# Performance work log

Measured on AMD Instinct MI355X. Metric: run time of the kernel, lower is better.

The kernel has to match this reference:

```python
import jax, jax.numpy as jnp
import numpy as np

B, T, D, N = 8, 2048, 1024, 256


def setup_inputs() -> dict:
    key = jax.random.key(0)
    ks = jax.random.split(key, 6)
    sD = 1.0 / np.sqrt(D)
    sN = 1.0 / np.sqrt(N)
    return {
        "x": jax.random.normal(ks[0], (B, T, D), dtype=jnp.float32),
        "Wa": jax.random.normal(ks[1], (D, N), dtype=jnp.float32) * sD,
        "ba": jnp.zeros((N,), jnp.float32),
        "Wb": jax.random.normal(ks[2], (D, N), dtype=jnp.float32) * sD,
        "bb": jnp.zeros((N,), jnp.float32),
        "Wc": jax.random.normal(ks[3], (D, N), dtype=jnp.float32) * sD,
        "bc": jnp.zeros((N,), jnp.float32),
        "Wd": jax.random.normal(ks[4], (D, D), dtype=jnp.float32) * sD,
        "bd": jnp.zeros((D,), jnp.float32),
        "Wy": jax.random.normal(ks[5], (N, D), dtype=jnp.float32) * sN,
        "by": jnp.zeros((D,), jnp.float32),
    }


def reference(x, Wa, ba, Wb, bb, Wc, bc, Wd, bd, Wy, by):
    # Precompute all input-dependent gates/projections in batched GEMMs.
    a = jax.nn.sigmoid(jnp.einsum("btd,dn->btn", x, Wa) + ba)  # (B,T,N)
    b = jnp.einsum("btd,dn->btn", x, Wb) + bb                   # (B,T,N)
    c = jnp.tanh(jnp.einsum("btd,dn->btn", x, Wc) + bc)          # (B,T,N)
    d = jnp.einsum("btd,de->bte", x, Wd) + bd                    # (B,T,D)

    # Sequential linear-gated recurrence: s_t = a_t*s_{t-1} + (1-a_t)*b_t
    def step(s, abc):
        at, bt, ct = abc
        s = at * s + (1.0 - at) * bt
        return s, ct * s

    aT = jnp.swapaxes(a, 0, 1)  # (T,B,N)
    bT = jnp.swapaxes(b, 0, 1)
    cT = jnp.swapaxes(c, 0, 1)
    s0 = jnp.zeros((x.shape[0], Wa.shape[1]), x.dtype)
    _, csT = jax.lax.scan(step, s0, (aT, bT, cT))  # (T,B,N)
    cs = jnp.swapaxes(csT, 0, 1)                    # (B,T,N)

    # Output projection applied once over the full sequence.
    y = jnp.einsum("btn,nd->btd", cs, Wy) + by + d  # (B,T,D)
    return y
```

## Files before the change

kernel.cpp:

```cpp
#include <hip/hip_runtime.h>
#include <hip/hip_bf16.h>

typedef unsigned short u16;
typedef __attribute__((ext_vector_type(8))) short bf16x8;
typedef __attribute__((ext_vector_type(4))) float f32x4;

#define AS1 __attribute__((address_space(1)))
#define AS3 __attribute__((address_space(3)))

#define Bx 8
#define Tt 2048
#define Dd 1024
#define Nn 256
#define Mm (Bx*Tt)
#define CHAINS (Bx*Nn)
#define NCH 32
#define TC 64
#define NCOMB 1792

#define WS_NEED 105644032u

#define CVT_BLOCKS (Mm*Dd/4/256)
#define PACK_BLOCKS (32*32*5)

__device__ __forceinline__ u16 f2bf(float f) {
  union { float f; unsigned u; } v; v.f = f;
  unsigned u = v.u;
  u += 0x7fffu + ((u >> 16) & 1u);
  return (u16)(u >> 16);
}

__device__ __forceinline__ float bf2f(u16 h) {
  union { unsigned u; float f; } v; v.u = ((unsigned)h) << 16;
  return v.f;
}

__device__ __forceinline__ void gload_lds16(const void* g, void* l) {
  __builtin_amdgcn_global_load_lds((AS1 void*)(g), (AS3 void*)(l), 16, 0, 0);
}

__global__ void prep_kernel(const float* __restrict__ x, u16* __restrict__ xb,
                            const float* __restrict__ Wa, const float* __restrict__ Wb,
                            const float* __restrict__ Wc, const float* __restrict__ Wd,
                            const float* __restrict__ Wy,
                            u16* __restrict__ Wcomb, u16* __restrict__ Wyt) {
  const int bid = blockIdx.x;
  if (bid < CVT_BLOCKS) {
    int i = bid * blockDim.x + threadIdx.x;
    float4 v = ((const float4*)x)[i];
    unsigned lo = (unsigned)f2bf(v.x) | ((unsigned)f2bf(v.y) << 16);
    unsigned hi = (unsigned)f2bf(v.z) | ((unsigned)f2bf(v.w) << 16);
    ((uint2*)xb)[i] = make_uint2(lo, hi);
    return;
  }
  __shared__ float tile[32][33];
  const int pid = bid - CVT_BLOCKS;
  const int z = pid >> 10;
  const int rem = pid & 1023;
  const int bx = rem & 31, by = rem >> 5;
  const float* src; u16* dst; int R, C, dld;
  if (z < 3)       { src = (z==0?Wa:(z==1?Wb:Wc)); dst = Wcomb + (size_t)z*256*1024; R=1024; C=256;  dld=1024; }
  else if (z == 3) { src = Wd; dst = Wcomb + (size_t)768*1024; R=1024; C=1024; dld=1024; }
  else             { src = Wy; dst = Wyt; R=256;  C=1024; dld=256;  }
  int c0 = bx * 32, r0 = by * 32;
  if (c0 >= C || r0 >= R) return;
  int tx = threadIdx.x & 31, ty = threadIdx.x >> 5;
  #pragma unroll
  for (int i = 0; i < 32; i += 8)
    tile[ty + i][tx] = src[(size_t)(r0 + ty + i)*C + (c0 + tx)];
  __syncthreads();
  #pragma unroll
  for (int i = 0; i < 32; i += 8) {
    int c = c0 + ty + i, r = r0 + tx;
    dst[(size_t)c*dld + r] = f2bf(tile[tx][ty + i]);
  }
}

template<int EPI>
__global__ __launch_bounds__(512, 4) void gemm_bt_kernel(
    const u16* __restrict__ A, const u16* __restrict__ Bt, int K, int gx,
    u16* __restrict__ outA, float* __restrict__ outO, u16* __restrict__ dtmp,
    const float* __restrict__ b0, const float* __restrict__ b1,
    const float* __restrict__ b2, const float* __restrict__ b3) {
  __shared__ u16 ldsA[256*64];
  __shared__ u16 ldsB[128*64];
  const int tid = threadIdx.x;
  const int lane = tid & 63, wid = tid >> 6;
  const int wm = wid >> 1, wn = wid & 1;

  const int h = blockIdx.x;
  const int id = (h & 7) * (gridDim.x >> 3) + (h >> 3);
  const int mt = id / gx, nt = id % gx;
  const int m0 = mt * 256, n0 = nt * 128;

  f32x4 acc[4][4] = {};

  const int rl  = tid >> 3;
  const int ssl = (tid & 7) ^ (rl & 7);

  auto stage = [&](int k0) {
    #pragma unroll
    for (int u = 0; u < 4; ++u)
      gload_lds16(A + (size_t)(m0 + u*64 + rl)*K + k0 + ssl*8,
                  ldsA + u*4096 + tid*8);
    #pragma unroll
    for (int u = 0; u < 2; ++u)
      gload_lds16(Bt + (size_t)(n0 + u*64 + rl)*K + k0 + ssl*8,
                  ldsB + u*4096 + tid*8);
  };

  const int lr = lane & 15, kq = lane >> 4, sw = lane & 7;
  const int arow = wm*64 + lr;
  const int brow = wn*64 + lr;

  for (int k0 = 0; k0 < K; k0 += 64) {
    stage(k0);
    __syncthreads();
    #pragma unroll
    for (int kk = 0; kk < 2; ++kk) {
      const int q = ((kk*4 + kq) ^ sw) * 8;
      bf16x8 af[4], bfr[4];
      #pragma unroll
      for (int mi = 0; mi < 4; ++mi)
        af[mi]  = *(const bf16x8*)&ldsA[(arow + mi*16)*64 + q];
      #pragma unroll
      for (int ni = 0; ni < 4; ++ni)
        bfr[ni] = *(const bf16x8*)&ldsB[(brow + ni*16)*64 + q];
      __builtin_amdgcn_s_setprio(1);
      #pragma unroll
      for (int mi = 0; mi < 4; ++mi)
        #pragma unroll
        for (int ni = 0; ni < 4; ++ni)
          acc[mi][ni] = __builtin_amdgcn_mfma_f32_16x16x32_bf16(af[mi], bfr[ni], acc[mi][ni], 0, 0, 0);
      __builtin_amdgcn_s_setprio(0);
    }
    __syncthreads();
  }

  const int crow = m0 + wm*64 + (lane >> 4)*4;
  const int ccol = wn*64 + (lane & 15);
  #pragma unroll
  for (int mi = 0; mi < 4; ++mi) {
    #pragma unroll
    for (int ni = 0; ni < 4; ++ni) {
      int coln = n0 + ccol + ni*16;
      #pragma unroll
      for (int r = 0; r < 4; ++r) {
        int row = crow + mi*16 + r;
        float v = acc[mi][ni][r];
        if (EPI == 0) {
          if (coln < 768) {
            int seg = coln >> 8, cn = coln & 255;
            if (seg == 0)      v = 1.f / (1.f + __expf(-(v + b0[cn])));
            else if (seg == 1) v = v + b1[cn];
            else               v = tanhf(v + b2[cn]);
            outA[(size_t)row*768 + coln] = f2bf(v);
          } else {
            int col = coln - 768;
            if (dtmp) dtmp[(size_t)row*1024 + col] = f2bf(v + b3[col]);
            else      outO[(size_t)row*1024 + col] = v + b3[col];
          }
        } else {
          const size_t o = (size_t)row*1024 + coln;
          if (dtmp) outO[o] = v + b0[coln] + bf2f(dtmp[o]);
          else      outO[o] = outO[o] + v + b0[coln];
        }
      }
    }
  }
}

__global__ void scanA_kernel(const u16* __restrict__ abc,
                             float* __restrict__ Asum, float* __restrict__ Usum) {
  int idx = blockIdx.x * blockDim.x + threadIdx.x;
  int chain = idx & (CHAINS - 1);
  int ch = idx >> 11;
  int bb = chain >> 8, n = chain & 255;
  const u16* base = abc + (size_t)(bb*Tt + ch*TC) * 768;
  float A = 1.f, U = 0.f;
  for (int t = 0; t < TC; ++t) {
    float a = bf2f(base[(size_t)t*768 + n]);
    float b = bf2f(base[(size_t)t*768 + 256 + n]);
    U = a*U + (1.f - a)*b;
    A *= a;
  }
  Asum[idx] = A; Usum[idx] = U;
}

__global__ void scanB_kernel(const float* __restrict__ Asum, const float* __restrict__ Usum,
                             float* __restrict__ Spre) {
  int chain = blockIdx.x * blockDim.x + threadIdx.x;
  float s = 0.f;
  for (int ch = 0; ch < NCH; ++ch) {
    int i = (ch << 11) + chain;
    Spre[i] = s;
    s = Asum[i]*s + Usum[i];
  }
}

__global__ void scanC_kernel(const u16* __restrict__ abc, const float* __restrict__ Spre,
                             u16* __restrict__ cs) {
  int idx = blockIdx.x * blockDim.x + threadIdx.x;
  int chain = idx & (CHAINS - 1);
  int ch = idx >> 11;
  int bb = chain >> 8, n = chain & 255;
  const u16* base = abc + (size_t)(bb*Tt + ch*TC) * 768;
  u16* csb = cs + (size_t)(bb*Tt + ch*TC) * 256 + n;
  float s = Spre[idx];
  for (int t = 0; t < TC; ++t) {
    float a = bf2f(base[(size_t)t*768 + n]);
    float b = bf2f(base[(size_t)t*768 + 256 + n]);
    float c = bf2f(base[(size_t)t*768 + 512 + n]);
    s = a*s + (1.f - a)*b;
    csb[(size_t)t*256] = f2bf(c*s);
  }
}

extern "C" void kernel_launch(void* const* d_in, const int* in_sizes, int n_in,
                              void* d_out, int out_size, void* d_ws, size_t ws_size,
                              hipStream_t stream) {
  const float* x  = (const float*)d_in[0];
  const float* Wa = (const float*)d_in[1];
  const float* ba = (const float*)d_in[2];
  const float* Wb = (const float*)d_in[3];
  const float* bb = (const float*)d_in[4];
  const float* Wc = (const float*)d_in[5];
  const float* bc = (const float*)d_in[6];
  const float* Wd = (const float*)d_in[7];
  const float* bd = (const float*)d_in[8];
  const float* Wy = (const float*)d_in[9];
  const float* by = (const float*)d_in[10];
  float* out = (float*)d_out;
  char* ws = (char*)d_ws;

  u16*  xb    = (u16*) (ws + 0);
  u16*  Wcomb = (u16*) (ws + 33554432);
  u16*  Wyt   = (u16*) (ws + 37224448);
  u16*  abcb  = (u16*) (ws + 37748736);
  u16*  cs    = (u16*) (ws + 62914560);
  float* Asum = (float*)(ws + 71303168);
  float* Usum = (float*)(ws + 71565312);
  float* Spre = (float*)(ws + 71827456);
  u16*  dtmp  = (ws_size >= WS_NEED) ? (u16*)(ws + 72089600) : nullptr;

  prep_kernel<<<CVT_BLOCKS + PACK_BLOCKS, 256, 0, stream>>>(
      x, xb, Wa, Wb, Wc, Wd, Wy, Wcomb, Wyt);
  gemm_bt_kernel<0><<<896, 512, 0, stream>>>(
      xb, Wcomb, Dd, NCOMB/128, abcb, out, dtmp, ba, bb, bc, bd);
  scanA_kernel<<<CHAINS*NCH/256, 256, 0, stream>>>(abcb, Asum, Usum);
  scanB_kernel<<<CHAINS/256, 256, 0, stream>>>(Asum, Usum, Spre);
  scanC_kernel<<<CHAINS*NCH/256, 256, 0, stream>>>(abcb, Spre, cs);
  gemm_bt_kernel<2><<<512, 512, 0, stream>>>(
      cs, Wyt, Nn, Dd/128, nullptr, out, dtmp, by, nullptr, nullptr, nullptr);
}
```

Before: 154.5 us.

## Double-buffer GEMM LDS tiles with 128x128 blocks and prefetch overlap

Block tiles in the bf16 GEMM shrink from 256x128 with 512 threads to 128x128 with 256 threads. LDS is double-buffered so the next K-slice is fetched by global_load_lds while MFMAs run on the current slice, and each iteration ends with explicit vmcnt waits and barriers. The goal is to hide global-load latency and cut the two syncthreads per K step. The cost is more blocks, which means more redundant B-tile traffic and a different occupancy mix.

```diff
diff --git a/kernel.cpp b/kernel.cpp
--- a/kernel.cpp
+++ b/kernel.cpp
@@ -22,6 +22,10 @@
 
 #define CVT_BLOCKS (Mm*Dd/4/256)
 #define PACK_BLOCKS (32*32*5)
+
+#define VMCNT0 asm volatile("s_waitcnt vmcnt(0)" ::: "memory")
+#define BARR   __builtin_amdgcn_s_barrier()
+#define SCHEDB __builtin_amdgcn_sched_barrier(0)
 
 __device__ __forceinline__ u16 f2bf(float f) {
   union { float f; unsigned u; } v; v.f = f;
@@ -77,55 +81,65 @@
 }
 
 template<int EPI>
-__global__ __launch_bounds__(512, 4) void gemm_bt_kernel(
+__global__ __launch_bounds__(256, 4) void gemm_bt_kernel(
     const u16* __restrict__ A, const u16* __restrict__ Bt, int K, int gx,
     u16* __restrict__ outA, float* __restrict__ outO, u16* __restrict__ dtmp,
     const float* __restrict__ b0, const float* __restrict__ b1,
     const float* __restrict__ b2, const float* __restrict__ b3) {
-  __shared__ u16 ldsA[256*64];
-  __shared__ u16 ldsB[128*64];
+  __shared__ u16 ldsA[2*128*64];
+  __shared__ u16 ldsB[2*128*64];
   const int tid = threadIdx.x;
   const int lane = tid & 63, wid = tid >> 6;
-  const int wm = wid >> 1, wn = wid & 1;
+  const int wr = wid >> 1, wc = wid & 1;
 
   const int h = blockIdx.x;
   const int id = (h & 7) * (gridDim.x >> 3) + (h >> 3);
   const int mt = id / gx, nt = id % gx;
-  const int m0 = mt * 256, n0 = nt * 128;
+  const int m0 = mt * 128, n0 = nt * 128;
+  const int NT = K >> 6;
 
   f32x4 acc[4][4] = {};
 
-  const int rl  = tid >> 3;
-  const int ssl = (tid & 7) ^ (rl & 7);
-
-  auto stage = [&](int k0) {
+  const int srow = lane >> 3;
+  const int sq   = (lane & 7) ^ srow;
+
+  auto stage = [&](int b, int t) {
+    const int k0 = t << 6;
     #pragma unroll
-    for (int u = 0; u < 4; ++u)
-      gload_lds16(A + (size_t)(m0 + u*64 + rl)*K + k0 + ssl*8,
-                  ldsA + u*4096 + tid*8);
-    #pragma unroll
-    for (int u = 0; u < 2; ++u)
-      gload_lds16(Bt + (size_t)(n0 + u*64 + rl)*K + k0 + ssl*8,
-                  ldsB + u*4096 + tid*8);
+    for (int i = 0; i < 4; ++i) {
+      int g = wid*4 + i;
+      int r = g*8 + srow;
+      gload_lds16(A + (size_t)(m0 + r)*K + k0 + sq*8, (char*)ldsA + b*16384 + g*1024);
+      gload_lds16(Bt + (size_t)(n0 + r)*K + k0 + sq*8, (char*)ldsB + b*16384 + g*1024);
+    }
   };
 
-  const int lr = lane & 15, kq = lane >> 4, sw = lane & 7;
-  const int arow = wm*64 + lr;
-  const int brow = wn*64 + lr;
-
-  for (int k0 = 0; k0 < K; k0 += 64) {
-    stage(k0);
-    __syncthreads();
+  const int kq  = lane >> 4;
+  const int swz = lane & 7;
+  const int arow = wr*64 + (lane & 15);
+  const int brow = wc*64 + (lane & 15);
+
+  stage(0, 0);
+  VMCNT0;
+  BARR; SCHEDB;
+
+  for (int t = 0; t < NT; ++t) {
+    const int cur = t & 1;
+    const int cb  = cur * 8192;
+
+    if (t + 1 < NT) stage(cur ^ 1, t + 1);
+    SCHEDB;
+
     #pragma unroll
     for (int kk = 0; kk < 2; ++kk) {
-      const int q = ((kk*4 + kq) ^ sw) * 8;
+      const int q = ((kk*4 + kq) ^ swz) * 8;
       bf16x8 af[4], bfr[4];
       #pragma unroll
       for (int mi = 0; mi < 4; ++mi)
-        af[mi]  = *(const bf16x8*)&ldsA[(arow + mi*16)*64 + q];
+        af[mi]  = *(const bf16x8*)&ldsA[cb + (arow + mi*16)*64 + q];
       #pragma unroll
       for (int ni = 0; ni < 4; ++ni)
-        bfr[ni] = *(const bf16x8*)&ldsB[(brow + ni*16)*64 + q];
+        bfr[ni] = *(const bf16x8*)&ldsB[cb + (brow + ni*16)*64 + q];
       __builtin_amdgcn_s_setprio(1);
       #pragma unroll
       for (int mi = 0; mi < 4; ++mi)
@@ -134,11 +148,13 @@
           acc[mi][ni] = __builtin_amdgcn_mfma_f32_16x16x32_bf16(af[mi], bfr[ni], acc[mi][ni], 0, 0, 0);
       __builtin_amdgcn_s_setprio(0);
     }
-    __syncthreads();
-  }
-
-  const int crow = m0 + wm*64 + (lane >> 4)*4;
-  const int ccol = wn*64 + (lane & 15);
+
+    VMCNT0;
+    BARR; SCHEDB;
+  }
+
+  const int crow = m0 + wr*64 + (lane >> 4)*4;
+  const int ccol = wc*64 + (lane & 15);
   #pragma unroll
   for (int mi = 0; mi < 4; ++mi) {
     #pragma unroll
@@ -245,11 +261,11 @@
 
   prep_kernel<<<CVT_BLOCKS + PACK_BLOCKS, 256, 0, stream>>>(
       x, xb, Wa, Wb, Wc, Wd, Wy, Wcomb, Wyt);
-  gemm_bt_kernel<0><<<896, 512, 0, stream>>>(
+  gemm_bt_kernel<0><<<1792, 256, 0, stream>>>(
       xb, Wcomb, Dd, NCOMB/128, abcb, out, dtmp, ba, bb, bc, bd);
   scanA_kernel<<<CHAINS*NCH/256, 256, 0, stream>>>(abcb, Asum, Usum);
   scanB_kernel<<<CHAINS/256, 256, 0, stream>>>(Asum, Usum, Spre);
   scanC_kernel<<<CHAINS*NCH/256, 256, 0, stream>>>(abcb, Spre, cs);
-  gemm_bt_kernel<2><<<512, 512, 0, stream>>>(
+  gemm_bt_kernel<2><<<1024, 256, 0, stream>>>(
       cs, Wyt, Nn, Dd/128, nullptr, out, dtmp, by, nullptr, nullptr, nullptr);
 }
```

New measurement: 208.1 us. +34.7%, slower.
